# Optimization experiments

Hardware: AMD Instinct MI355X
Metric: run time of the kernel (lower is better)

## Reference

```python
import jax, jax.numpy as jnp
import numpy as np

NUM_HEADS = 16
EPS = 1e-5


def setup_inputs() -> dict:
    key = jax.random.key(0)
    ks = jax.random.split(key, 9)
    B, S, D = 2, 2048, 1024
    s = 1.0 / np.sqrt(D)
    return {
        "x": jax.random.normal(ks[0], (B, S, D), dtype=jnp.float32),
        "Wq": jax.random.uniform(ks[1], (D, D), jnp.float32, -s, s),
        "bq": jax.random.uniform(ks[2], (D,), jnp.float32, -s, s),
        "Wk": jax.random.uniform(ks[3], (D, D), jnp.float32, -s, s),
        "bk": jax.random.uniform(ks[4], (D,), jnp.float32, -s, s),
        "Wv": jax.random.uniform(ks[5], (D, D), jnp.float32, -s, s),
        "bv": jax.random.uniform(ks[6], (D,), jnp.float32, -s, s),
        "Wo": jax.random.uniform(ks[7], (D, D), jnp.float32, -s, s),
        "bo": jax.random.uniform(ks[8], (D,), jnp.float32, -s, s),
    }


def reference(x, Wq, bq, Wk, bk, Wv, bv, Wo, bo):
    B, S, D = x.shape
    H = NUM_HEADS
    hd = D // H
    # projections -> [B, H, S, hd]
    def proj(W, b):
        return (x @ W + b).reshape(B, S, H, hd).transpose(0, 2, 1, 3)
    Q = proj(Wq, bq)
    K = proj(Wk, bk)
    V = proj(Wv, bv)
    scores = jnp.einsum("bhqd,bhkd->bhqk", Q, K) / jnp.sqrt(jnp.float32(hd))
    attn = jax.nn.softmax(scores, axis=-1)  # dropout is identity in eval mode
    out = jnp.einsum("bhqk,bhkd->bhqd", attn, V)
    out = out.transpose(0, 2, 1, 3).reshape(B, S, D)
    out = jax.nn.relu(out @ Wo + bo)
    mu = jnp.mean(out, axis=-1, keepdims=True)
    var = jnp.var(out, axis=-1, keepdims=True)
    return (out - mu) * jax.lax.rsqrt(var + EPS)
```

## Files before the change

kernel.cpp:

```cpp
#include <hip/hip_runtime.h>
#include <hip/hip_bf16.h>
#include <math.h>

#define Bb 2
#define Ss 2048
#define Dd 1024
#define Hh 16
#define HD 64
#define Mm (Bb*Ss)

typedef __attribute__((ext_vector_type(8))) short bf8_t;
typedef __attribute__((ext_vector_type(4))) float f4_t;
typedef __attribute__((ext_vector_type(4))) unsigned u4_t;
typedef __attribute__((ext_vector_type(2))) unsigned uint2v;

#define LOG2E 1.4426950408889634f

#define AS1 __attribute__((address_space(1)))
#define AS3 __attribute__((address_space(3)))

__device__ __forceinline__ void gl2lds16(const void* g, void* l) {
    __builtin_amdgcn_global_load_lds((const AS1 unsigned int*)g,
                                     (AS3 unsigned int*)l, 16, 0, 0);
}
__device__ __forceinline__ short bfr(float f) {
    __hip_bfloat16 h = __float2bfloat16(f);
    return *reinterpret_cast<short*>(&h);
}
__device__ __forceinline__ unsigned pkbf16(float a, float b) {
    const unsigned ua = __builtin_bit_cast(unsigned, a) + 0x8000u;
    const unsigned ub = __builtin_bit_cast(unsigned, b) + 0x8000u;
    return __builtin_amdgcn_perm(ub, ua, 0x07060302u);
}
__device__ __forceinline__ float fexp2(float x) {
    return __builtin_amdgcn_exp2f(x);
}
__device__ __forceinline__ float b2f(unsigned short u) {
    return __builtin_bit_cast(float, (unsigned)u << 16);
}
__device__ __forceinline__ void pl32(unsigned &a, unsigned &b) {
#if __has_builtin(__builtin_amdgcn_permlane32_swap)
    uint2v r = __builtin_amdgcn_permlane32_swap(a, b, false, false);
    a = r[0]; b = r[1];
#else
    asm volatile("v_permlane32_swap_b32 %0, %1" : "+v"(a), "+v"(b));
#endif
}
__device__ __forceinline__ void pl16(unsigned &a, unsigned &b) {
#if __has_builtin(__builtin_amdgcn_permlane16_swap)
    uint2v r = __builtin_amdgcn_permlane16_swap(a, b, false, false);
    a = r[0]; b = r[1];
#else
    asm volatile("v_permlane16_swap_b32 %0, %1" : "+v"(a), "+v"(b));
#endif
}

__global__ __launch_bounds__(256)
void prep(const float* __restrict__ x,
          const float* __restrict__ w0, const float* __restrict__ w1,
          const float* __restrict__ w2, const float* __restrict__ w3,
          __hip_bfloat16* __restrict__ Wt4, __hip_bfloat16* __restrict__ Xh)
{
    const int z = blockIdx.z;
    if (z < 4) {
        const float* W = (z == 0) ? w0 : (z == 1) ? w1 : (z == 2) ? w2 : w3;
        __hip_bfloat16* Wt = Wt4 + (size_t)z * Dd * Dd;
        __shared__ float t[32][33];
        const int n0 = blockIdx.x * 32, k0 = blockIdx.y * 32;
        const int tx = threadIdx.x & 31, ty = threadIdx.x >> 5;
        #pragma unroll
        for (int rr = 0; rr < 4; ++rr)
            t[ty + rr*8][tx] = W[(size_t)(k0 + ty + rr*8) * Dd + n0 + tx];
        __syncthreads();
        #pragma unroll
        for (int rr = 0; rr < 4; ++rr)
            Wt[(size_t)(n0 + ty + rr*8) * Dd + k0 + tx] =
                __float2bfloat16(t[tx][ty + rr*8]);
    } else {
        const int bid = (z - 4) * 1024 + blockIdx.y * 32 + blockIdx.x;
        const size_t i = ((size_t)bid * 256 + threadIdx.x) * 8;
        const float4 a = *(const float4*)&x[i];
        const float4 b = *(const float4*)&x[i + 4];
        bf8_t o;
        o[0] = bfr(a.x); o[1] = bfr(a.y); o[2] = bfr(a.z); o[3] = bfr(a.w);
        o[4] = bfr(b.x); o[5] = bfr(b.y); o[6] = bfr(b.z); o[7] = bfr(b.w);
        *(bf8_t*)&Xh[i] = o;
    }
}

__global__ __launch_bounds__(256)
void gemm_qkv(const __hip_bfloat16* __restrict__ A,
              const __hip_bfloat16* __restrict__ Bt,
              const float* __restrict__ b0, const float* __restrict__ b1,
              const float* __restrict__ b2,
              __hip_bfloat16* __restrict__ Qh, __hip_bfloat16* __restrict__ Kh,
              __hip_bfloat16* __restrict__ Vt)
{
    __shared__ __align__(16) char pool[34816];
    __hip_bfloat16* As = (__hip_bfloat16*)pool;
    __hip_bfloat16* Bs = As + 2 * 128 * 32;

    const int lin  = blockIdx.y * 24 + blockIdx.x;
    const int xcd  = lin & 7;
    const int idx  = lin >> 3;
    const int by   = (xcd >> 1) * 8 + idx / 12;
    const int bx   = (xcd & 1) * 12 + idx % 12;

    const int tid  = threadIdx.x;
    const int wave = tid >> 6;
    const int lane = tid & 63;
    const int llo  = lane & 15;
    const int lhi  = lane >> 4;
    const int wm   = wave & 1;
    const int wn   = wave >> 1;
    const int row0 = by * 128;
    const int col0 = bx * 128;

    size_t aoff[2], boff[2];
    int    loff[2];
    #pragma unroll
    for (int p = 0; p < 2; ++p) {
        const int g = p * 256 + wave * 64 + lane;
        const int r = g >> 2;
        const int kc = ((g & 3) ^ ((r >> 1) & 3)) * 8;
        aoff[p] = (size_t)(row0 + r) * Dd + kc;
        boff[p] = (size_t)(col0 + r) * Dd + kc;
        loff[p] = (p * 256 + wave * 64) * 16;
    }
    const __hip_bfloat16* Acur = A;
    const __hip_bfloat16* Bcur = Bt;

    auto stage = [&](int buf) {
        #pragma unroll
        for (int p = 0; p < 2; ++p) {
            gl2lds16(Acur + aoff[p], (char*)As + buf*8192 + loff[p]);
            gl2lds16(Bcur + boff[p], (char*)Bs + buf*8192 + loff[p]);
        }
        Acur += 32; Bcur += 32;
    };

    const int xch = (lhi ^ ((llo >> 1) & 3)) * 8;

    f4_t acc[4][4] = {};
    stage(0);
    for (int kt = 0; kt < 32; ++kt) {
        const int buf = kt & 1;
        __syncthreads();
        if (kt + 1 < 32) stage(buf ^ 1);

        bf8_t a[4], b[4];
        #pragma unroll
        for (int i = 0; i < 4; ++i)
            a[i] = *(const bf8_t*)&As[buf*4096 + (wm*64 + i*16 + llo) * 32 + xch];
        #pragma unroll
        for (int j = 0; j < 4; ++j)
            b[j] = *(const bf8_t*)&Bs[buf*4096 + (wn*64 + j*16 + llo) * 32 + xch];
        #pragma unroll
        for (int i = 0; i < 4; ++i)
            #pragma unroll
            for (int j = 0; j < 4; ++j)
                acc[i][j] = __builtin_amdgcn_mfma_f32_16x16x32_bf16(
                    a[i], b[j], acc[i][j], 0, 0, 0);
    }

    const int sel   = col0 >> 10;
    const int cbase = col0 & 1023;
    __hip_bfloat16* Ls = (__hip_bfloat16*)pool;
    __syncthreads();

    float bv[4];
    const float* bp = (sel == 0) ? b0 : (sel == 1) ? b1 : b2;
    #pragma unroll
    for (int j = 0; j < 4; ++j) bv[j] = bp[cbase + wn*64 + j*16 + llo];
    const float scale = (sel == 0) ? 0.125f * LOG2E : 1.0f;

    if (sel < 2) {
        #pragma unroll
        for (int i = 0; i < 4; ++i)
            #pragma unroll
            for (int r = 0; r < 4; ++r) {
                const int ml = wm*64 + i*16 + lhi*4 + r;
                #pragma unroll
                for (int j = 0; j < 4; ++j)
                    Ls[ml*136 + wn*64 + j*16 + llo] =
                        __float2bfloat16((acc[i][j][r] + bv[j]) * scale);
            }
        __syncthreads();
        __hip_bfloat16* outQK = (sel == 0) ? Qh : Kh;
        #pragma unroll
        for (int p = 0; p < 8; ++p) {
            const int id = p*256 + tid;
            const int rl = id >> 4;
            const int c8 = (id & 15) * 8;
            const bf8_t v = *(const bf8_t*)&Ls[rl*136 + c8];
            const int m  = row0 + rl;
            const int b_ = m >> 11, s_ = m & (Ss - 1);
            const int col = cbase + c8;
            *(bf8_t*)&outQK[((size_t)(b_*Hh + (col >> 6))*Ss + s_)*HD + (col & 63)] = v;
        }
    } else {
        #pragma unroll
        for (int i = 0; i < 4; ++i)
            #pragma unroll
            for (int r = 0; r < 4; ++r) {
                const int ml = wm*64 + i*16 + lhi*4 + r;
                #pragma unroll
                for (int j = 0; j < 4; ++j)
                    Ls[(wn*64 + j*16 + llo)*136 + ml] =
                        __float2bfloat16(acc[i][j][r] + bv[j]);
            }
        __syncthreads();
        const int b_ = row0 >> 11;
        const int sb = row0 & (Ss - 1);
        #pragma unroll
        for (int p = 0; p < 8; ++p) {
            const int cl = p*16 + (tid >> 4);
            const int m  = (tid & 15) * 8;
            const bf8_t v = *(const bf8_t*)&Ls[cl*136 + m];
            const int cc = cbase + cl;
            *(bf8_t*)&Vt[((size_t)(b_*Hh + (cc >> 6))*HD + (cc & 63))*Ss + sb + m] = v;
        }
    }
}

__global__ __launch_bounds__(256, 2)
void attn_mfma(const __hip_bfloat16* __restrict__ Qh,
               const __hip_bfloat16* __restrict__ Kh,
               const __hip_bfloat16* __restrict__ Vt,
               __hip_bfloat16* __restrict__ Ah)
{
    const int lin  = (blockIdx.z * Hh + blockIdx.y) * (Ss/128) + blockIdx.x;
    const int xcd  = lin & 7;
    const int slot = lin >> 3;
    const int grp  = (xcd << 2) | (slot >> 4);
    const int qc   = slot & 15;
    const int b    = grp >> 4;
    const int h    = grp & 15;

    const int wave = threadIdx.x >> 6;
    const int lane = threadIdx.x & 63;
    const int llo  = lane & 15;
    const int lhi  = lane >> 4;
    const int qb   = qc * 128 + wave * 32;

    const size_t base = ((size_t)(b*Hh + h)) * Ss * HD;

    __shared__ __hip_bfloat16 Ks[2][2 * 64 * 32];
    __shared__ __hip_bfloat16 Vs[2][2 * 64 * 32];

    int koff[2], voff[2], loff[2];
    #pragma unroll
    for (int it = 0; it < 2; ++it) {
        const int g  = it*256 + wave*64 + lane;
        const int hf = g >> 8;
        const int rr = (g >> 2) & 63;
        const int c8 = ((g & 3) ^ ((rr >> 1) & 3)) * 8;
        koff[it] = rr*HD + hf*32 + c8;
        voff[it] = rr*Ss + hf*32 + c8;
        loff[it] = (it*256 + wave*64) * 16;
    }
    const __hip_bfloat16* Kcur = Kh + base;
    const __hip_bfloat16* Vcur = Vt + base;

    auto stage = [&](int buf) {
        #pragma unroll
        for (int it = 0; it < 2; ++it) {
            gl2lds16(Kcur + koff[it], (char*)&Ks[buf][0] + loff[it]);
            gl2lds16(Vcur + voff[it], (char*)&Vs[buf][0] + loff[it]);
        }
        Kcur += 64 * HD;
        Vcur += 64;
    };

    bf8_t qf[2][2];
    #pragma unroll
    for (int s = 0; s < 2; ++s)
        #pragma unroll
        for (int d = 0; d < 2; ++d)
            qf[s][d] = *(const bf8_t*)&Qh[base + (size_t)(qb + 16*s + llo)*HD + 32*d + lhi*8];

    f4_t o_[2][4];
    f4_t lsum[2];
    #pragma unroll
    for (int s = 0; s < 2; ++s) {
        #pragma unroll
        for (int n = 0; n < 4; ++n) o_[s][n] = (f4_t){0.f,0.f,0.f,0.f};
        lsum[s] = (f4_t){0.f,0.f,0.f,0.f};
    }
    const short oneb = 0x3F80;
    const bf8_t vones = {oneb,oneb,oneb,oneb,oneb,oneb,oneb,oneb};

    const f4_t zf = {0.f,0.f,0.f,0.f};
    const int xch = (lhi ^ ((llo >> 1) & 3)) * 8;

    bf8_t pfp[2][2];
    bf8_t vfp[4][2];

    stage(0);

    for (int t = 0; t < Ss/64; ++t) {
        const int buf = t & 1;
        __syncthreads();
        if (t + 1 < Ss/64) stage(buf ^ 1);

        bf8_t kf[4][2];
        #pragma unroll
        for (int kc = 0; kc < 4; ++kc)
            #pragma unroll
            for (int d = 0; d < 2; ++d)
                kf[kc][d] = *(const bf8_t*)&Ks[buf][d*2048 + (kc*16 + llo)*32 + xch];

        f4_t sacc[2][4];
        #pragma unroll
        for (int s = 0; s < 2; ++s)
            #pragma unroll
            for (int kc = 0; kc < 4; ++kc) {
                sacc[s][kc] = __builtin_amdgcn_mfma_f32_16x16x32_bf16(kf[kc][0], qf[s][0], zf, 0, 0, 0);
                sacc[s][kc] = __builtin_amdgcn_mfma_f32_16x16x32_bf16(kf[kc][1], qf[s][1], sacc[s][kc], 0, 0, 0);
            }

        if (t > 0) {
            __builtin_amdgcn_s_setprio(1);
            #pragma unroll
            for (int d = 0; d < 2; ++d)
                #pragma unroll
                for (int nc = 0; nc < 4; ++nc)
                    #pragma unroll
                    for (int s = 0; s < 2; ++s)
                        o_[s][nc] = __builtin_amdgcn_mfma_f32_16x16x32_bf16(pfp[s][d], vfp[nc][d], o_[s][nc], 0, 0, 0);
            #pragma unroll
            for (int s = 0; s < 2; ++s)
                #pragma unroll
                for (int d = 0; d < 2; ++d)
                    lsum[s] = __builtin_amdgcn_mfma_f32_16x16x32_bf16(pfp[s][d], vones, lsum[s], 0, 0, 0);
            __builtin_amdgcn_s_setprio(0);
        }

        #pragma unroll
        for (int nc = 0; nc < 4; ++nc)
            #pragma unroll
            for (int d = 0; d < 2; ++d)
                vfp[nc][d] = *(const bf8_t*)&Vs[buf][d*2048 + (nc*16 + llo)*32 + xch];

        #pragma unroll
        for (int s = 0; s < 2; ++s) {
            unsigned w[4][2];
            #pragma unroll
            for (int kc = 0; kc < 4; ++kc) {
                const float p0 = fexp2(sacc[s][kc][0]);
                const float p1 = fexp2(sacc[s][kc][1]);
                const float p2 = fexp2(sacc[s][kc][2]);
                const float p3 = fexp2(sacc[s][kc][3]);
                w[kc][0] = pkbf16(p0, p1);
                w[kc][1] = pkbf16(p2, p3);
            }
            #pragma unroll
            for (int d = 0; d < 2; ++d) {
                u4_t pu;
                #pragma unroll
                for (int hh = 0; hh < 2; ++hh) {
                    unsigned U = w[2*d][hh], V = w[2*d+1][hh];
                    pl32(U, V);
                    pl16(U, V);
                    pu[hh]     = U;
                    pu[2 + hh] = V;
                }
                pfp[s][d] = __builtin_bit_cast(bf8_t, pu);
            }
        }
    }

    #pragma unroll
    for (int d = 0; d < 2; ++d)
        #pragma unroll
        for (int nc = 0; nc < 4; ++nc)
            #pragma unroll
            for (int s = 0; s < 2; ++s)
                o_[s][nc] = __builtin_amdgcn_mfma_f32_16x16x32_bf16(pfp[s][d], vfp[nc][d], o_[s][nc], 0, 0, 0);
    #pragma unroll
    for (int s = 0; s < 2; ++s)
        #pragma unroll
        for (int d = 0; d < 2; ++d)
            lsum[s] = __builtin_amdgcn_mfma_f32_16x16x32_bf16(pfp[s][d], vones, lsum[s], 0, 0, 0);

    #pragma unroll
    for (int s = 0; s < 2; ++s) {
        #pragma unroll
        for (int r = 0; r < 4; ++r) {
            const float inv = 1.0f / lsum[s][r];
            const int q = qb + 16*s + 4*lhi + r;
            __hip_bfloat16* orow = &Ah[((size_t)(b*Ss) + q)*Dd + h*HD + llo];
            #pragma unroll
            for (int nc = 0; nc < 4; ++nc)
                orow[16*nc] = __float2bfloat16(o_[s][nc][r] * inv);
        }
    }
}

__global__ __launch_bounds__(256)
void gemm_out(const __hip_bfloat16* __restrict__ A,
              const __hip_bfloat16* __restrict__ Bt,
              const float* __restrict__ bias,
              __hip_bfloat16* __restrict__ R)
{
    __shared__ __align__(16) char pool[24576];
    __hip_bfloat16* As = (__hip_bfloat16*)pool;
    __hip_bfloat16* Bs = As + 2 * 128 * 32;

    const int lin = blockIdx.y * 16 + blockIdx.x;
    const int xcd = lin & 7;
    const int idx = lin >> 3;
    const int by  = (xcd >> 1) * 8 + (idx >> 3);
    const int bx  = (xcd & 1) * 8 + (idx & 7);

    const int tid  = threadIdx.x;
    const int wave = tid >> 6;
    const int lane = tid & 63;
    const int llo  = lane & 15;
    const int lhi  = lane >> 4;
    const int wm   = wave & 1;
    const int wn   = wave >> 1;
    const int row0 = by * 128;
    const int col0 = bx * 64;

    size_t aoff[2], boff;
    int    loffA[2], loffB;
    #pragma unroll
    for (int p = 0; p < 2; ++p) {
        const int g = p * 256 + wave * 64 + lane;
        const int r = g >> 2;
        const int kc = ((g & 3) ^ ((r >> 1) & 3)) * 8;
        aoff[p]  = (size_t)(row0 + r) * Dd + kc;
        loffA[p] = (p * 256 + wave * 64) * 16;
    }
    {
        const int g = wave * 64 + lane;
        const int r = g >> 2;
        const int kc = ((g & 3) ^ ((r >> 1) & 3)) * 8;
        boff  = (size_t)(col0 + r) * Dd + kc;
        loffB = (wave * 64) * 16;
    }
    const __hip_bfloat16* Acur = A;
    const __hip_bfloat16* Bcur = Bt;

    auto stage = [&](int buf) {
        #pragma unroll
        for (int p = 0; p < 2; ++p)
            gl2lds16(Acur + aoff[p], (char*)As + buf*8192 + loffA[p]);
        gl2lds16(Bcur + boff, (char*)Bs + buf*4096 + loffB);
        Acur += 32; Bcur += 32;
    };

    const int xch = (lhi ^ ((llo >> 1) & 3)) * 8;

    f4_t acc[4][2] = {};
    stage(0);
    for (int kt = 0; kt < 32; ++kt) {
        const int buf = kt & 1;
        __syncthreads();
        if (kt + 1 < 32) stage(buf ^ 1);

        bf8_t a[4], b[2];
        #pragma unroll
        for (int i = 0; i < 4; ++i)
            a[i] = *(const bf8_t*)&As[buf*4096 + (wm*64 + i*16 + llo) * 32 + xch];
        #pragma unroll
        for (int j = 0; j < 2; ++j)
            b[j] = *(const bf8_t*)&Bs[buf*2048 + (wn*32 + j*16 + llo) * 32 + xch];
        #pragma unroll
        for (int i = 0; i < 4; ++i)
            #pragma unroll
            for (int j = 0; j < 2; ++j)
                acc[i][j] = __builtin_amdgcn_mfma_f32_16x16x32_bf16(
                    a[i], b[j], acc[i][j], 0, 0, 0);
    }

    __hip_bfloat16* Ls = (__hip_bfloat16*)pool;
    __syncthreads();

    float bv[2];
    #pragma unroll
    for (int j = 0; j < 2; ++j) bv[j] = bias[col0 + wn*32 + j*16 + llo];

    #pragma unroll
    for (int i = 0; i < 4; ++i)
        #pragma unroll
        for (int r = 0; r < 4; ++r) {
            const int ml = wm*64 + i*16 + lhi*4 + r;
            #pragma unroll
            for (int j = 0; j < 2; ++j)
                Ls[ml*72 + wn*32 + j*16 + llo] =
                    __float2bfloat16(fmaxf(acc[i][j][r] + bv[j], 0.0f));
        }
    __syncthreads();
    #pragma unroll
    for (int p = 0; p < 4; ++p) {
        const int id = p*256 + tid;
        const int rl = id >> 3;
        const int c8 = (id & 7) * 8;
        const bf8_t v = *(const bf8_t*)&Ls[rl*72 + c8];
        *(bf8_t*)&R[(size_t)(row0 + rl)*Dd + col0 + c8] = v;
    }
}

__global__ __launch_bounds__(256)
void layernorm(const __hip_bfloat16* __restrict__ R, float* __restrict__ out)
{
    const int row = blockIdx.x;
    const int c = threadIdx.x;
    const ushort4 a = ((const ushort4*)(R + (size_t)row*Dd))[c];
    float4 v;
    v.x = b2f(a.x); v.y = b2f(a.y); v.z = b2f(a.z); v.w = b2f(a.w);

    float s  = v.x + v.y + v.z + v.w;
    float ss = v.x*v.x + v.y*v.y + v.z*v.z + v.w*v.w;
    #pragma unroll
    for (int off = 32; off > 0; off >>= 1) {
        s  += __shfl_down(s,  off);
        ss += __shfl_down(ss, off);
    }
    __shared__ float rs[4], rss[4];
    const int wid = c >> 6, lid = c & 63;
    if (lid == 0) { rs[wid] = s; rss[wid] = ss; }
    __syncthreads();
    s  = rs[0] + rs[1] + rs[2] + rs[3];
    ss = rss[0] + rss[1] + rss[2] + rss[3];
    const float mean = s * (1.0f / Dd);
    const float var  = ss * (1.0f / Dd) - mean * mean;
    const float rstd = rsqrtf(var + 1e-5f);
    float4 o;
    o.x = (v.x - mean) * rstd;
    o.y = (v.y - mean) * rstd;
    o.z = (v.z - mean) * rstd;
    o.w = (v.w - mean) * rstd;
    ((float4*)(out + (size_t)row*Dd))[c] = o;
}

extern "C" void kernel_launch(void* const* d_in, const int* in_sizes, int n_in,
                              void* d_out, int out_size, void* d_ws, size_t ws_size,
                              hipStream_t stream)
{
    const float* x  = (const float*)d_in[0];
    const float* Wq = (const float*)d_in[1];
    const float* bq = (const float*)d_in[2];
    const float* Wk = (const float*)d_in[3];
    const float* bk = (const float*)d_in[4];
    const float* Wv = (const float*)d_in[5];
    const float* bv = (const float*)d_in[6];
    const float* Wo = (const float*)d_in[7];
    const float* bo = (const float*)d_in[8];
    float* out = (float*)d_out;

    __hip_bfloat16* Xh    = (__hip_bfloat16*)d_ws;
    __hip_bfloat16* Wqkvt = Xh    + (size_t)Mm*Dd;
    __hip_bfloat16* Wot   = Wqkvt + (size_t)3*Dd*Dd;
    __hip_bfloat16* Ah    = Wot   + (size_t)Dd*Dd;
    __hip_bfloat16* Qh    = Ah    + (size_t)Mm*Dd;
    __hip_bfloat16* Kh    = Qh    + (size_t)Mm*Dd;
    __hip_bfloat16* Vt    = Kh    + (size_t)Mm*Dd;
    __hip_bfloat16* Rb    = Qh;

    prep<<<dim3(32, 32, 6), dim3(256), 0, stream>>>(x, Wq, Wk, Wv, Wo, Wqkvt, Xh);
    gemm_qkv<<<dim3(3*Dd/128, Mm/128), dim3(256), 0, stream>>>(
        Xh, Wqkvt, bq, bk, bv, Qh, Kh, Vt);
    attn_mfma<<<dim3(Ss/128, Hh, Bb), dim3(256), 0, stream>>>(Qh, Kh, Vt, Ah);
    gemm_out<<<dim3(Dd/64, Mm/128), dim3(256), 0, stream>>>(Ah, Wot, bo, Rb);
    layernorm<<<dim3(Mm), dim3(256), 0, stream>>>(Rb, out);
}
```

Before: 189.1 us.

## Enlarge QKV GEMM tiles to 256x256 with triple-buffered async LDS pipeline

The QKV projection GEMM moves from 128x128 tiles with 256 threads and double buffering to 256x256 tiles with 512 threads, a three-stage global-to-LDS pipeline, split half-stage prefetches interleaved with MFMA phases, and raised wave priority during MFMA. The epilogue writes through XOR-swizzled per-wave LDS regions in two rounds to scatter Q/K and the transposed V. The aim is more operand reuse per loaded byte and better overlap of loads with matrix math. In exchange the grid shrinks to 192 blocks, which may underfill the device's compute units. The larger LDS footprint and register accumulators also limit occupancy.

```diff
diff --git a/kernel.cpp b/kernel.cpp
--- a/kernel.cpp
+++ b/kernel.cpp
@@ -88,7 +88,7 @@
     }
 }
 
-__global__ __launch_bounds__(256)
+__global__ __launch_bounds__(512)
 void gemm_qkv(const __hip_bfloat16* __restrict__ A,
               const __hip_bfloat16* __restrict__ Bt,
               const float* __restrict__ b0, const float* __restrict__ b1,
@@ -96,130 +96,174 @@
               __hip_bfloat16* __restrict__ Qh, __hip_bfloat16* __restrict__ Kh,
               __hip_bfloat16* __restrict__ Vt)
 {
-    __shared__ __align__(16) char pool[34816];
-    __hip_bfloat16* As = (__hip_bfloat16*)pool;
-    __hip_bfloat16* Bs = As + 2 * 128 * 32;
-
-    const int lin  = blockIdx.y * 24 + blockIdx.x;
-    const int xcd  = lin & 7;
-    const int idx  = lin >> 3;
-    const int by   = (xcd >> 1) * 8 + idx / 12;
-    const int bx   = (xcd & 1) * 12 + idx % 12;
+    __shared__ __align__(16) char pool[98304];
+
+    const int lin = blockIdx.y * 12 + blockIdx.x;
+    const int xcd = lin & 7;
+    const int idx = lin >> 3;
+    const int by  = (xcd >> 1) * 4 + idx / 6;
+    const int bx  = (xcd & 1) * 6 + idx % 6;
 
     const int tid  = threadIdx.x;
     const int wave = tid >> 6;
     const int lane = tid & 63;
     const int llo  = lane & 15;
     const int lhi  = lane >> 4;
-    const int wm   = wave & 1;
-    const int wn   = wave >> 1;
-    const int row0 = by * 128;
-    const int col0 = bx * 128;
-
-    size_t aoff[2], boff[2];
-    int    loff[2];
-    #pragma unroll
-    for (int p = 0; p < 2; ++p) {
-        const int g = p * 256 + wave * 64 + lane;
-        const int r = g >> 2;
-        const int kc = ((g & 3) ^ ((r >> 1) & 3)) * 8;
-        aoff[p] = (size_t)(row0 + r) * Dd + kc;
-        boff[p] = (size_t)(col0 + r) * Dd + kc;
-        loff[p] = (p * 256 + wave * 64) * 16;
-    }
-    const __hip_bfloat16* Acur = A;
-    const __hip_bfloat16* Bcur = Bt;
-
-    auto stage = [&](int buf) {
-        #pragma unroll
-        for (int p = 0; p < 2; ++p) {
-            gl2lds16(Acur + aoff[p], (char*)As + buf*8192 + loff[p]);
-            gl2lds16(Bcur + boff[p], (char*)Bs + buf*8192 + loff[p]);
-        }
-        Acur += 32; Bcur += 32;
+    const int wm   = wave >> 2;
+    const int wn   = wave & 3;
+    const int row0 = by * 256;
+    const int col0 = bx * 256;
+
+    const int g0 = tid,        r0 = g0 >> 2;
+    const int g1 = 512 + tid,  r1 = g1 >> 2;
+    const int kc0 = ((g0 & 3) ^ ((r0 >> 1) & 3)) * 8;
+    const int kc1 = ((g1 & 3) ^ ((r1 >> 1) & 3)) * 8;
+    const size_t aO0 = (size_t)(row0 + r0) * Dd + kc0;
+    const size_t aO1 = (size_t)(row0 + r1) * Dd + kc1;
+    const size_t bO0 = (size_t)(col0 + r0) * Dd + kc0;
+    const size_t bO1 = (size_t)(col0 + r1) * Dd + kc1;
+    const int ldsOff0 = (wave * 64) * 16;
+    const int ldsOff1 = (512 + wave * 64) * 16;
+
+    auto stageH = [&](int kt, int h) {
+        const int s = kt % 3;
+        const size_t ko = (size_t)kt * 32;
+        if (h == 0) {
+            gl2lds16(A  + aO0 + ko, pool + s*16384 + ldsOff0);
+            gl2lds16(Bt + bO0 + ko, pool + 49152 + s*16384 + ldsOff0);
+        } else {
+            gl2lds16(A  + aO1 + ko, pool + s*16384 + ldsOff1);
+            gl2lds16(Bt + bO1 + ko, pool + 49152 + s*16384 + ldsOff1);
+        }
     };
 
     const int xch = (lhi ^ ((llo >> 1) & 3)) * 8;
 
-    f4_t acc[4][4] = {};
-    stage(0);
+    f4_t acc[8][4] = {};
+
+    stageH(0, 0); stageH(0, 1);
+    stageH(1, 0); stageH(1, 1);
+    asm volatile("s_waitcnt vmcnt(4)" ::: "memory");
+    __builtin_amdgcn_s_barrier();
+    __builtin_amdgcn_sched_barrier(0);
+
     for (int kt = 0; kt < 32; ++kt) {
-        const int buf = kt & 1;
-        __syncthreads();
-        if (kt + 1 < 32) stage(buf ^ 1);
-
-        bf8_t a[4], b[4];
+        const int s_ = kt % 3;
+        const __hip_bfloat16* As_s = (const __hip_bfloat16*)(pool + s_*16384);
+        const __hip_bfloat16* Bs_s = (const __hip_bfloat16*)(pool + 49152 + s_*16384);
+        const bool st = (kt < 30);
+
+        bf8_t b_[4], a_[4];
+        #pragma unroll
+        for (int j = 0; j < 4; ++j)
+            b_[j] = *(const bf8_t*)&Bs_s[(wn*64 + j*16 + llo) * 32 + xch];
         #pragma unroll
         for (int i = 0; i < 4; ++i)
-            a[i] = *(const bf8_t*)&As[buf*4096 + (wm*64 + i*16 + llo) * 32 + xch];
-        #pragma unroll
-        for (int j = 0; j < 4; ++j)
-            b[j] = *(const bf8_t*)&Bs[buf*4096 + (wn*64 + j*16 + llo) * 32 + xch];
+            a_[i] = *(const bf8_t*)&As_s[(wm*128 + i*16 + llo) * 32 + xch];
+        if (st) stageH(kt + 2, 0);
+        __builtin_amdgcn_s_barrier();
+        __builtin_amdgcn_s_setprio(1);
         #pragma unroll
         for (int i = 0; i < 4; ++i)
             #pragma unroll
             for (int j = 0; j < 4; ++j)
                 acc[i][j] = __builtin_amdgcn_mfma_f32_16x16x32_bf16(
-                    a[i], b[j], acc[i][j], 0, 0, 0);
+                    a_[i], b_[j], acc[i][j], 0, 0, 0);
+        __builtin_amdgcn_s_setprio(0);
+        __builtin_amdgcn_s_barrier();
+
+        #pragma unroll
+        for (int i = 0; i < 4; ++i)
+            a_[i] = *(const bf8_t*)&As_s[(wm*128 + (i+4)*16 + llo) * 32 + xch];
+        if (st) stageH(kt + 2, 1);
+        __builtin_amdgcn_s_barrier();
+        __builtin_amdgcn_s_setprio(1);
+        #pragma unroll
+        for (int i = 0; i < 4; ++i)
+            #pragma unroll
+            for (int j = 0; j < 4; ++j)
+                acc[i+4][j] = __builtin_amdgcn_mfma_f32_16x16x32_bf16(
+                    a_[i], b_[j], acc[i+4][j], 0, 0, 0);
+        __builtin_amdgcn_s_setprio(0);
+
+        if (st) asm volatile("s_waitcnt vmcnt(4)" ::: "memory");
+        else    asm volatile("s_waitcnt vmcnt(0)" ::: "memory");
+        __builtin_amdgcn_s_barrier();
+        __builtin_amdgcn_sched_barrier(0);
     }
 
     const int sel   = col0 >> 10;
     const int cbase = col0 & 1023;
-    __hip_bfloat16* Ls = (__hip_bfloat16*)pool;
+    const int headc = (cbase >> 6) + wn;
+    const float* bp = (sel == 0) ? b0 : (sel == 1) ? b1 : b2;
+    float bvv[4];
+    #pragma unroll
+    for (int j = 0; j < 4; ++j) bvv[j] = bp[cbase + wn*64 + j*16 + llo];
+    const float scale = (sel == 0) ? 0.125f * LOG2E : 1.0f;
+    const int mbase = row0 + wm*128;
+    const int b_i   = mbase >> 11;
+    const int s0_   = mbase & (Ss - 1);
+
     __syncthreads();
-
-    float bv[4];
-    const float* bp = (sel == 0) ? b0 : (sel == 1) ? b1 : b2;
-    #pragma unroll
-    for (int j = 0; j < 4; ++j) bv[j] = bp[cbase + wn*64 + j*16 + llo];
-    const float scale = (sel == 0) ? 0.125f * LOG2E : 1.0f;
-
-    if (sel < 2) {
-        #pragma unroll
-        for (int i = 0; i < 4; ++i)
-            #pragma unroll
-            for (int r = 0; r < 4; ++r) {
-                const int ml = wm*64 + i*16 + lhi*4 + r;
+    __hip_bfloat16* Ls = (__hip_bfloat16*)(pool + wn*16384);
+
+    #pragma unroll
+    for (int round = 0; round < 2; ++round) {
+        if (wm == round) {
+            if (sel < 2) {
                 #pragma unroll
-                for (int j = 0; j < 4; ++j)
-                    Ls[ml*136 + wn*64 + j*16 + llo] =
-                        __float2bfloat16((acc[i][j][r] + bv[j]) * scale);
+                for (int i = 0; i < 8; ++i)
+                    #pragma unroll
+                    for (int r = 0; r < 4; ++r) {
+                        const int rr = i*16 + lhi*4 + r;
+                        #pragma unroll
+                        for (int j = 0; j < 4; ++j) {
+                            const int cc = j*16 + llo;
+                            Ls[rr*64 + (((cc >> 3) ^ (rr & 7)) << 3) + (cc & 7)] =
+                                __float2bfloat16((acc[i][j][r] + bvv[j]) * scale);
+                        }
+                    }
+            } else {
+                #pragma unroll
+                for (int i = 0; i < 8; ++i)
+                    #pragma unroll
+                    for (int r = 0; r < 4; ++r) {
+                        const int rr = i*16 + lhi*4 + r;
+                        #pragma unroll
+                        for (int j = 0; j < 4; ++j) {
+                            const int cc = j*16 + llo;
+                            Ls[cc*128 + (((rr >> 3) ^ (cc & 15)) << 3) + (rr & 7)] =
+                                __float2bfloat16(acc[i][j][r] + bvv[j]);
+                        }
+                    }
             }
+        }
         __syncthreads();
-        __hip_bfloat16* outQK = (sel == 0) ? Qh : Kh;
-        #pragma unroll
-        for (int p = 0; p < 8; ++p) {
-            const int id = p*256 + tid;
-            const int rl = id >> 4;
-            const int c8 = (id & 15) * 8;
-            const bf8_t v = *(const bf8_t*)&Ls[rl*136 + c8];
-            const int m  = row0 + rl;
-            const int b_ = m >> 11, s_ = m & (Ss - 1);
-            const int col = cbase + c8;
-            *(bf8_t*)&outQK[((size_t)(b_*Hh + (col >> 6))*Ss + s_)*HD + (col & 63)] = v;
-        }
-    } else {
-        #pragma unroll
-        for (int i = 0; i < 4; ++i)
-            #pragma unroll
-            for (int r = 0; r < 4; ++r) {
-                const int ml = wm*64 + i*16 + lhi*4 + r;
+        if (wm == round) {
+            if (sel < 2) {
+                __hip_bfloat16* outQK = (sel == 0) ? Qh : Kh;
+                __hip_bfloat16* ob = outQK + (size_t)(b_i*Hh + headc) * Ss * HD;
                 #pragma unroll
-                for (int j = 0; j < 4; ++j)
-                    Ls[(wn*64 + j*16 + llo)*136 + ml] =
-                        __float2bfloat16(acc[i][j][r] + bv[j]);
+                for (int t = 0; t < 16; ++t) {
+                    const int id = t*64 + lane;
+                    const int rr = id >> 3;
+                    const int cq = id & 7;
+                    const bf8_t v = *(const bf8_t*)&Ls[rr*64 + ((cq ^ (rr & 7)) << 3)];
+                    *(bf8_t*)&ob[(size_t)(s0_ + rr)*HD + cq*8] = v;
+                }
+            } else {
+                __hip_bfloat16* vb = Vt + (size_t)(b_i*Hh + headc) * HD * Ss;
+                #pragma unroll
+                for (int t = 0; t < 16; ++t) {
+                    const int id = t*64 + lane;
+                    const int hd = id >> 4;
+                    const int mc = id & 15;
+                    const bf8_t v = *(const bf8_t*)&Ls[hd*128 + ((mc ^ (hd & 15)) << 3)];
+                    *(bf8_t*)&vb[(size_t)hd*Ss + s0_ + mc*8] = v;
+                }
             }
+        }
         __syncthreads();
-        const int b_ = row0 >> 11;
-        const int sb = row0 & (Ss - 1);
-        #pragma unroll
-        for (int p = 0; p < 8; ++p) {
-            const int cl = p*16 + (tid >> 4);
-            const int m  = (tid & 15) * 8;
-            const bf8_t v = *(const bf8_t*)&Ls[cl*136 + m];
-            const int cc = cbase + cl;
-            *(bf8_t*)&Vt[((size_t)(b_*Hh + (cc >> 6))*HD + (cc & 63))*Ss + sb + m] = v;
-        }
     }
 }
 
@@ -561,7 +605,7 @@
     __hip_bfloat16* Rb    = Qh;
 
     prep<<<dim3(32, 32, 6), dim3(256), 0, stream>>>(x, Wq, Wk, Wv, Wo, Wqkvt, Xh);
-    gemm_qkv<<<dim3(3*Dd/128, Mm/128), dim3(256), 0, stream>>>(
+    gemm_qkv<<<dim3(3*Dd/256, Mm/256), dim3(512), 0, stream>>>(
         Xh, Wqkvt, bq, bk, bv, Qh, Kh, Vt);
     attn_mfma<<<dim3(Ss/128, Hh, Bb), dim3(256), 0, stream>>>(Qh, Kh, Vt, Ah);
     gemm_out<<<dim3(Dd/64, Mm/128), dim3(256), 0, stream>>>(Ah, Wot, bo, Rb);
```

Measured after the change: 191.7 us. No clear change (+1.4%).
